# Performance work log

Measured on AMD Instinct MI355X. Metric: run time of the kernel, lower is better.

The kernel has to match this reference:

```python
import jax, jax.numpy as jnp
import numpy as np

B = 64; C = 64; DIN = 512; F = 16; S = 2; C1O = 32; C2O = 64; ND2 = 27; FC1O = 512
D = 64; CL1_F = 64; CL1_K = 5; CL2_F = 128; CL2_K = 5; FC1_F = 512; FC2_F = 2; P = 2
FC1FIN = CL2_F * (D // (P * P))  # 2048


def _conv1d(x, w, b):
    # x [B, Cin, L], w [Cout, Cin, F] -> valid conv, stride S
    y = jax.lax.conv_general_dilated(x, w, (S,), 'VALID', dimension_numbers=('NCH', 'OIH', 'NCH'))
    return y + b[None, :, None]


def _bn_c(x, g, b, eps):
    # BatchNorm1d on [B, Ch, L]: normalize each channel over (B, L) (training-mode batch stats)
    m = x.mean((0, 2), keepdims=True)
    v = ((x - m) ** 2).mean((0, 2), keepdims=True)
    return (x - m) * jax.lax.rsqrt(v + eps) * g[None, :, None] + b[None, :, None]


def _pool(x, p=2):
    # MaxPool1d(p) over last dim, floor division like torch
    L = x.shape[-1]; l = L // p
    return x[..., :l * p].reshape(x.shape[:-1] + (l, p)).max(-1)


def _branch(xc, w1, b1, g1, be1, w2, b2, g2, be2, lw, lb):
    # xc [B, 1, DIN] -> [B, FC1O]; matches max_pool(bn(relu(conv(x))), 2) twice + relu(lin1)
    o = _pool(_bn_c(jnp.maximum(_conv1d(xc, w1, b1), 0.0), g1, be1, 1e-5))
    o = _pool(_bn_c(jnp.maximum(_conv1d(o, w2, b2), 0.0), g2, be2, 1e-5))
    o = o.reshape(o.shape[0], -1)
    return jnp.maximum(o @ lw.T + lb, 0.0)


def _cheby(x, Lm, lmax, W, b, K):
    # x [B, V, Fin]; Chebyshev recursion x_k = 2 L~ x_{k-1} - x_{k-2}
    Bx, V, Fin = x.shape
    Lr = 2.0 * Lm / lmax - jnp.eye(V, dtype=x.dtype)  # rescale_L
    x0 = x.transpose(1, 2, 0).reshape(V, Fin * Bx)
    xs = [x0]
    x1 = Lr @ x0
    xs.append(x1)
    for _ in range(2, K):
        x2 = 2.0 * (Lr @ x1) - x0
        xs.append(x2)
        x0, x1 = x1, x2
    Xk = jnp.stack(xs).reshape(K, V, Fin, Bx).transpose(3, 1, 2, 0).reshape(Bx * V, Fin * K)
    return (Xk @ W.T + b).reshape(Bx, V, -1)


def _gbn(x, g, b, eps):
    # BatchNorm1d(V, eps) on [B, V, F]: per-node stats over (B, F). eps is CL1_F/CL2_F (bug in source, kept faithful)
    m = x.mean((0, 2), keepdims=True)
    v = ((x - m) ** 2).mean((0, 2), keepdims=True)
    return (x - m) * jax.lax.rsqrt(v + eps) * g[None, :, None] + b[None, :, None]


def _gpool(x):
    # graph_max_pool p=2 over node dim
    Bx, V, Fo = x.shape
    return x.reshape(Bx, V // 2, 2, Fo).max(2)


def _forward(inp, L0, L1, conv1_w, conv1_b, bn1_g, bn1_b, conv2_w, conv2_b, bn2_g, bn2_b,
             lin1_w, lin1_b, cl1_w, cl1_b, gbn1_g, gbn1_b, cl2_w, cl2_b, gbn2_g, gbn2_b,
             fc1_w, fc1_b, fc2_w, fc2_b, perm, lmax0, lmax1):
    xc = inp.transpose(1, 0, 2)[:, :, None, :]  # [C, B, 1, DIN]
    cout = jax.vmap(_branch)(xc, conv1_w, conv1_b, bn1_g, bn1_b,
                             conv2_w, conv2_b, bn2_g, bn2_b, lin1_w, lin1_b)  # [C, B, FC1O]
    x = cout[perm].transpose(1, 0, 2)  # perm_data + permute -> [B, D, FC1O]
    x = _cheby(x, L0, float(lmax0), cl1_w, cl1_b, CL1_K)
    x = _gbn(jnp.maximum(x, 0.0), gbn1_g, gbn1_b, float(CL1_F))
    x = _gpool(x)  # [B, D//2, CL1_F]
    x = _cheby(x, L1, float(lmax1), cl2_w, cl2_b, CL2_K)
    x = _gbn(jnp.maximum(x, 0.0), gbn2_g, gbn2_b, float(CL2_F))
    x = _gpool(x)  # [B, D//4, CL2_F]
    x = x.reshape(-1, FC1FIN)
    x = jnp.maximum(x @ fc1_w.T + fc1_b, 0.0)
    # Dropout(d) with d=0 is identity
    return x @ fc2_w.T + fc2_b  # [B, FC2_F]


def setup_inputs() -> dict:
    key = jax.random.key(0)
    ks = jax.random.split(key, 12)
    n = lambda k, shp: jax.random.normal(k, shp, jnp.float32) * 0.02
    A0 = jax.random.normal(ks[0], (D, D), jnp.float32); L0 = (A0 + A0.T) / 2.0
    A1 = jax.random.normal(ks[1], (D // 2, D // 2), jnp.float32); L1 = (A1 + A1.T) / 2.0
    return dict(
        inp=jax.random.normal(ks[2], (B, C, DIN), jnp.float32),
        d=0, L0=L0, L1=L1, lmax0=2, lmax1=2,
        perm=jnp.arange(D, dtype=jnp.int32), epoch_num=0,
        conv1_w=n(ks[3], (C, C1O, 1, F)), conv1_b=jnp.zeros((C, C1O), jnp.float32),
        bn1_g=jnp.ones((C, C1O), jnp.float32), bn1_b=jnp.zeros((C, C1O), jnp.float32),
        conv2_w=n(ks[4], (C, C2O, C1O, F)), conv2_b=jnp.zeros((C, C2O), jnp.float32),
        bn2_g=jnp.ones((C, C2O), jnp.float32), bn2_b=jnp.zeros((C, C2O), jnp.float32),
        lin1_w=n(ks[5], (C, FC1O, C2O * ND2)), lin1_b=jnp.zeros((C, FC1O), jnp.float32),
        cl1_w=n(ks[6], (CL1_F, CL1_K * FC1O)), cl1_b=jnp.zeros((CL1_F,), jnp.float32),
        gbn1_g=jnp.ones((D,), jnp.float32), gbn1_b=jnp.zeros((D,), jnp.float32),
        cl2_w=n(ks[7], (CL2_F, CL2_K * CL1_F)), cl2_b=jnp.zeros((CL2_F,), jnp.float32),
        gbn2_g=jnp.ones((D // 2,), jnp.float32), gbn2_b=jnp.zeros((D // 2,), jnp.float32),
        fc1_w=n(ks[8], (FC1_F, FC1FIN)), fc1_b=jnp.zeros((FC1_F,), jnp.float32),
        fc2_w=n(ks[9], (FC2_F, FC1_F)), fc2_b=jnp.zeros((FC2_F,), jnp.float32))


def reference(inp, d, L0, L1, lmax0, lmax1, perm, epoch_num,
              conv1_w, conv1_b, bn1_g, bn1_b, conv2_w, conv2_b, bn2_g, bn2_b,
              lin1_w, lin1_b, cl1_w, cl1_b, gbn1_g, gbn1_b, cl2_w, cl2_b, gbn2_g, gbn2_b,
              fc1_w, fc1_b, fc2_w, fc2_b):
    return _forward(inp, L0, L1, conv1_w, conv1_b, bn1_g, bn1_b, conv2_w, conv2_b, bn2_g, bn2_b,
                    lin1_w, lin1_b, cl1_w, cl1_b, gbn1_g, gbn1_b, cl2_w, cl2_b, gbn2_g, gbn2_b,
                    fc1_w, fc1_b, fc2_w, fc2_b, perm, lmax0, lmax1)
```

## Files before the change

### kernel.cpp

```cpp
#include <hip/hip_runtime.h>
#include <hip/hip_bf16.h>

typedef __attribute__((ext_vector_type(8))) short short8;
typedef __attribute__((ext_vector_type(4))) float f32x4;

namespace {
constexpr int Bn  = 64;
constexpr int Cn  = 64;
constexpr int C1O = 32, C2O = 64;
constexpr int L1O = 249, L1P = 124;
constexpr int L2O = 55,  L2P = 27;
constexpr int FIN1 = 512;
constexpr int LIN1K = C2O * L2P;

constexpr long S1S = 0;
constexpr long S1Q = 2048;
constexpr long S2S = 4096;
constexpr long S2Q = 8192;

constexpr long LR0_B  = 65536;
constexpr long LR1_B  = 81920;
constexpr long W1RB_B = 86016;
constexpr long W2RB_B = 413696;
constexpr long W2B_B  = 495616;
constexpr long P1B_B  = 4689920;
constexpr long Y2_B   = 37195776;
constexpr long QB_B   = 94867456;
constexpr long CO_B   = 109023232;
constexpr long XK_B   = 4689920;
constexpr long CH1_B  = 117411840;
constexpr long X2K_B  = 118460416;
constexpr long CH2_B  = 118984704;
constexpr long FCI_B  = 120033280;
constexpr long FO1_B  = 120295424;
}

__device__ __forceinline__ unsigned short f2bf(float f) {
    union { float f; unsigned u; } v; v.f = f;
    unsigned r = v.u + 0x7FFFu + ((v.u >> 16) & 1u);
    return (unsigned short)(r >> 16);
}
__device__ __forceinline__ float bf2f(unsigned short s) {
    union { unsigned u; float f; } v; v.u = ((unsigned)s) << 16;
    return v.f;
}
__device__ __forceinline__ short8 cvt8(float4 a, float4 b) {
    float f[8] = {a.x, a.y, a.z, a.w, b.x, b.y, b.z, b.w};
    union { unsigned short s[8]; short8 v; } r;
#pragma unroll
    for (int i = 0; i < 8; ++i) r.s[i] = f2bf(f[i]);
    return r.v;
}
__device__ __forceinline__ uint2 pack4(float4 a) {
    union { unsigned short s[4]; uint2 u; } r;
    r.s[0] = f2bf(a.x); r.s[1] = f2bf(a.y); r.s[2] = f2bf(a.z); r.s[3] = f2bf(a.w);
    return r.u;
}

__global__ void prep_kernel(const float* __restrict__ L0, const float* __restrict__ L1m,
                            const int* __restrict__ lmax0, const int* __restrict__ lmax1,
                            const float* __restrict__ cl1w, const float* __restrict__ cl2w,
                            const float* __restrict__ conv2w, float* __restrict__ ws)
{
    long idx = (long)blockIdx.x * 256 + threadIdx.x;
    float inv0 = 2.0f / (float)lmax0[0];
    float inv1 = 2.0f / (float)lmax1[0];
    char* wsb = (char*)ws;
    float* LR0p = (float*)(wsb + LR0_B);
    float* LR1p = (float*)(wsb + LR1_B);
    unsigned short* W1Rp = (unsigned short*)(wsb + W1RB_B);
    unsigned short* W2Rp = (unsigned short*)(wsb + W2RB_B);
    unsigned short* w2b  = (unsigned short*)(wsb + W2B_B);
    if (idx < 12288) {
        ws[idx] = 0.f;
    } else if (idx < 12288 + 4096) {
        long t = idx - 12288; int i = t / 64, j = t % 64;
        LR0p[t] = L0[t] * inv0 - (i == j ? 1.0f : 0.0f);
    } else if (idx < 12288 + 4096 + 1024) {
        long t = idx - 12288 - 4096; int i = t / 32, j = t % 32;
        LR1p[t] = L1m[t] * inv1 - (i == j ? 1.0f : 0.0f);
    } else if (idx < 12288 + 4096 + 1024 + 163840) {
        long t = idx - 12288 - 4096 - 1024;
        int k = t / 32768; int r = t % 32768; int o = r / 512, f = r % 512;
        W1Rp[t] = f2bf(cl1w[o * 2560 + f * 5 + k]);
    } else if (idx < 12288 + 4096 + 1024 + 163840 + 40960) {
        long t = idx - 12288 - 4096 - 1024 - 163840;
        int k = t / 8192; int r = t % 8192; int o = r / 64, f = r % 64;
        W2Rp[t] = f2bf(cl2w[o * 320 + f * 5 + k]);
    } else if (idx < 12288 + 4096 + 1024 + 163840 + 40960 + 2097152) {
        long t = idx - 12288 - 4096 - 1024 - 163840 - 40960;
        w2b[t] = f2bf(conv2w[t]);
    }
}

__global__ __launch_bounds__(256) void conv1_p1_kernel(const float* __restrict__ inp,
    const float* __restrict__ w1, const float* __restrict__ b1, float* __restrict__ ws)
{
    int c = blockIdx.x >> 3, bg = blockIdx.x & 7;
    __shared__ float xs[8][512];
    __shared__ float rs[8][32], rq[8][32];
    int tid = threadIdx.x;
#pragma unroll
    for (int it = 0; it < 4; ++it) {
        int f4 = it * 256 + tid;
        int bl = f4 >> 7, off = (f4 & 127) * 4;
        *(float4*)&xs[bl][off] = *(const float4*)&inp[((long)(bg * 8 + bl) * 64 + c) * 512 + off];
    }
    int o = tid & 31, bq = tid >> 5;
    int co = c * 32 + o;
    float w[16];
#pragma unroll
    for (int t = 0; t < 16; ++t) w[t] = w1[co * 16 + t];
    float bias = b1[co];
    __syncthreads();
    float s = 0.f, q = 0.f;
    for (int jg = 0; jg < 31; ++jg) {
        float x[32];
#pragma unroll
        for (int h = 0; h < 8; ++h) *(float4*)&x[h * 4] = *(const float4*)&xs[bq][jg * 16 + h * 4];
#pragma unroll
        for (int j = 0; j < 8; ++j) {
            float a = bias;
#pragma unroll
            for (int t = 0; t < 16; ++t) a = fmaf(x[2 * j + t], w[t], a);
            a = fmaxf(a, 0.f);
            s += a; q += a * a;
        }
    }
    {
        float x[16];
#pragma unroll
        for (int h = 0; h < 4; ++h) *(float4*)&x[h * 4] = *(const float4*)&xs[bq][496 + h * 4];
        float a = bias;
#pragma unroll
        for (int t = 0; t < 16; ++t) a = fmaf(x[t], w[t], a);
        a = fmaxf(a, 0.f);
        s += a; q += a * a;
    }
    rs[bq][o] = s; rq[bq][o] = q;
    __syncthreads();
    if (tid < 32) {
        float ss = 0.f, qq = 0.f;
#pragma unroll
        for (int i = 0; i < 8; ++i) { ss += rs[i][tid]; qq += rq[i][tid]; }
        atomicAdd(&ws[S1S + c * 32 + tid], ss);
        atomicAdd(&ws[S1Q + c * 32 + tid], qq);
    }
}

__global__ __launch_bounds__(256) void conv1_p2_kernel(const float* __restrict__ inp,
    const float* __restrict__ w1, const float* __restrict__ b1,
    const float* __restrict__ g, const float* __restrict__ be,
    const float* __restrict__ ws, unsigned short* __restrict__ p1)
{
    int c = blockIdx.x >> 3, bg = blockIdx.x & 7;
    __shared__ float xs[8][512];
    int tid = threadIdx.x;
#pragma unroll
    for (int it = 0; it < 4; ++it) {
        int f4 = it * 256 + tid;
        int bl = f4 >> 7, off = (f4 & 127) * 4;
        *(float4*)&xs[bl][off] = *(const float4*)&inp[((long)(bg * 8 + bl) * 64 + c) * 512 + off];
    }
    int o = tid & 31, bq = tid >> 5;
    int co = c * 32 + o;
    float w[16];
#pragma unroll
    for (int t = 0; t < 16; ++t) w[t] = w1[co * 16 + t];
    float bias = b1[co];
    float N = (float)(Bn * L1O);
    float m = ws[S1S + co] / N;
    float inv = rsqrtf(ws[S1Q + co] / N - m * m + 1e-5f);
    float sc = inv * g[co], sh = be[co] - m * sc;
    __syncthreads();
    unsigned short* op = p1 + ((long)(c * 64 + bg * 8 + bq) * 32 + o) * 124;
    for (int jg = 0; jg < 31; ++jg) {
        float x[32];
#pragma unroll
        for (int h = 0; h < 8; ++h) *(float4*)&x[h * 4] = *(const float4*)&xs[bq][jg * 16 + h * 4];
        union { unsigned short r[4]; uint2 u; } pk;
#pragma unroll
        for (int p = 0; p < 4; ++p) {
            float a0 = bias, a1 = bias;
#pragma unroll
            for (int t = 0; t < 16; ++t) {
                a0 = fmaf(x[4 * p + t], w[t], a0);
                a1 = fmaf(x[4 * p + 2 + t], w[t], a1);
            }
            float v0 = fmaxf(a0, 0.f) * sc + sh;
            float v1 = fmaxf(a1, 0.f) * sc + sh;
            pk.r[p] = f2bf(fmaxf(v0, v1));
        }
        *(uint2*)&op[jg * 4] = pk.u;
    }
}

__global__ __launch_bounds__(256) void conv2_mfma_kernel(const unsigned short* __restrict__ p1b,
    const unsigned short* __restrict__ w2b, const float* __restrict__ b2,
    unsigned short* __restrict__ y2b, float* __restrict__ s2s, float* __restrict__ s2q)
{
    int c = blockIdx.y;
    int m0 = blockIdx.x * 128;
    __shared__ unsigned short Bl[64 * 512];
    __shared__ float red[2][4][64];
    int tid = threadIdx.x;
    int w = tid >> 6, lane = tid & 63;
    int lx = lane & 15, g = lane >> 4;

    const unsigned short* wsrc = w2b + (long)c * 32768;
#pragma unroll
    for (int it = 0; it < 16; ++it) {
        int j = it * 256 + tid;
        int n = j >> 6, kb = j & 63;
        uint4 val = *(const uint4*)(wsrc + n * 512 + kb * 8);
        int dst = (n * 1024 + kb * 16) ^ ((n & 7) << 4);
        *(uint4*)((char*)Bl + dst) = val;
    }
    __syncthreads();

    const unsigned short* abase[2];
#pragma unroll
    for (int ma = 0; ma < 2; ++ma) {
        int m = m0 + w * 32 + ma * 16 + lx;
        m = min(m, 3519);
        int b = m / 55, lp = m % 55;
        abase[ma] = p1b + ((long)(c * 64 + b) * 32) * 124 + 2 * lp + (g & 1) * 8;
    }
    int cio = g >> 1;

    f32x4 acc[2][4] = {};
    for (int kstep = 0; kstep < 16; ++kstep) {
        short8 af[2];
#pragma unroll
        for (int ma = 0; ma < 2; ++ma) {
            const unsigned short* ap = abase[ma] + (kstep * 2 + cio) * 124;
            union { unsigned u[4]; short8 v; } t;
            t.u[0] = *(const unsigned*)(ap + 0);
            t.u[1] = *(const unsigned*)(ap + 2);
            t.u[2] = *(const unsigned*)(ap + 4);
            t.u[3] = *(const unsigned*)(ap + 6);
            af[ma] = t.v;
        }
#pragma unroll
        for (int fi = 0; fi < 4; ++fi) {
            int n = fi * 16 + lx;
            int off = (n * 1024 + kstep * 64 + g * 16) ^ ((n & 7) << 4);
            short8 bfrag = *(const short8*)((char*)Bl + off);
#pragma unroll
            for (int ma = 0; ma < 2; ++ma)
                acc[ma][fi] = __builtin_amdgcn_mfma_f32_16x16x32_bf16(af[ma], bfrag, acc[ma][fi], 0, 0, 0);
        }
    }

    float cs[4] = {}, cq[4] = {};
#pragma unroll
    for (int fi = 0; fi < 4; ++fi) {
        int o2 = fi * 16 + lx;
        float bia = b2[c * 64 + o2];
#pragma unroll
        for (int ma = 0; ma < 2; ++ma) {
#pragma unroll
            for (int r = 0; r < 4; ++r) {
                int mm = m0 + w * 32 + ma * 16 + g * 4 + r;
                if (mm < 3520) {
                    int bb = mm / 55, ll = mm % 55;
                    float y = fmaxf(acc[ma][fi][r] + bia, 0.f);
                    y2b[((long)(c * 64 + bb) * 55 + ll) * 64 + o2] = f2bf(y);
                    cs[fi] += y; cq[fi] += y * y;
                }
            }
        }
    }
#pragma unroll
    for (int fi = 0; fi < 4; ++fi) {
        cs[fi] += __shfl_xor(cs[fi], 16); cs[fi] += __shfl_xor(cs[fi], 32);
        cq[fi] += __shfl_xor(cq[fi], 16); cq[fi] += __shfl_xor(cq[fi], 32);
    }
    __syncthreads();
    if (g == 0) {
#pragma unroll
        for (int fi = 0; fi < 4; ++fi) { red[0][w][fi * 16 + lx] = cs[fi]; red[1][w][fi * 16 + lx] = cq[fi]; }
    }
    __syncthreads();
    if (tid < 64) {
        float ss = red[0][0][tid] + red[0][1][tid] + red[0][2][tid] + red[0][3][tid];
        float qq = red[1][0][tid] + red[1][1][tid] + red[1][2][tid] + red[1][3][tid];
        atomicAdd(&s2s[c * 64 + tid], ss);
        atomicAdd(&s2q[c * 64 + tid], qq);
    }
}

__global__ __launch_bounds__(256) void bn2_pool_kernel(const unsigned short* __restrict__ y2b,
    const float* __restrict__ ws, const float* __restrict__ g, const float* __restrict__ be,
    unsigned short* __restrict__ q)
{
    int bid = blockIdx.x;
// ... 91 lines not shown
        float acc[8][4] = {};
        for (int u = 0; u < 64; ++u) {
            float4 xv = *(const float4*)&prev[u][cg * 4];
            float4 l0 = *(const float4*)&Lt[u * 64 + vg * 8];
            float4 l1 = *(const float4*)&Lt[u * 64 + vg * 8 + 4];
            float lv[8] = {l0.x, l0.y, l0.z, l0.w, l1.x, l1.y, l1.z, l1.w};
#pragma unroll
            for (int i = 0; i < 8; ++i) {
                acc[i][0] = fmaf(lv[i], xv.x, acc[i][0]);
                acc[i][1] = fmaf(lv[i], xv.y, acc[i][1]);
                acc[i][2] = fmaf(lv[i], xv.z, acc[i][2]);
                acc[i][3] = fmaf(lv[i], xv.w, acc[i][3]);
            }
        }
#pragma unroll
        for (int i = 0; i < 8; ++i) {
            int v = vg * 8 + i;
            float4 r;
            if (k == 1) {
                r.x = acc[i][0]; r.y = acc[i][1]; r.z = acc[i][2]; r.w = acc[i][3];
            } else {
                float4 p = *(const float4*)&dst[v][cg * 4];
                r.x = 2.f * acc[i][0] - p.x; r.y = 2.f * acc[i][1] - p.y;
                r.z = 2.f * acc[i][2] - p.z; r.w = 2.f * acc[i][3] - p.w;
            }
            *(float4*)&dst[v][cg * 4] = r;
            *(uint2*)&xkb[(long)k * 2097152 + (long)v * 32768 + col] = pack4(r);
        }
        __syncthreads();
    }
}

__global__ __launch_bounds__(256) void cheby1_mfma_kernel(const unsigned short* __restrict__ xkb,
    const unsigned short* __restrict__ w1rb, const float* __restrict__ bias, float* __restrict__ out)
{
    int m0 = blockIdx.x * 16;
    __shared__ unsigned short Bl[64 * 512];
    int tid = threadIdx.x, wv = tid >> 6, lane = tid & 63;
    int lx = lane & 15, g = lane >> 4;
    int m = m0 + lx;
    int v = m & 63, b = m >> 6;

    f32x4 acc = {};
    for (int kc = 0; kc < 5; ++kc) {
        __syncthreads();
#pragma unroll
        for (int it = 0; it < 16; ++it) {
            int j = it * 256 + tid;
            int n = j >> 6, kb = j & 63;
            uint4 val = *(const uint4*)(w1rb + (long)kc * 32768 + n * 512 + kb * 8);
            int dst = (n * 1024 + kb * 16) ^ ((n & 7) << 4);
            *(uint4*)((char*)Bl + dst) = val;
        }
        __syncthreads();
        const unsigned short* ab = xkb + (long)(kc * 64 + v) * 32768 + b * 512 + g * 8;
        for (int kl = 0; kl < 16; ++kl) {
            short8 af = *(const short8*)(ab + kl * 32);
            int n = wv * 16 + lx;
            int off = (n * 1024 + kl * 64 + g * 16) ^ ((n & 7) << 4);
            short8 bfrag = *(const short8*)((char*)Bl + off);
            acc = __builtin_amdgcn_mfma_f32_16x16x32_bf16(af, bfrag, acc, 0, 0, 0);
        }
    }
    int o = wv * 16 + lx;
    float bia = bias[o];
#pragma unroll
    for (int r = 0; r < 4; ++r) {
        int mm = m0 + g * 4 + r;
        int vv = mm & 63, bb = mm >> 6;
        out[((long)(bb * 64 + vv)) * 64 + o] = fmaxf(acc[r] + bia, 0.f);
    }
}

template<int Fdim, int XOUT>
__global__ __launch_bounds__(256) void gbn_gpool_kernel(const float* __restrict__ y,
    const float* __restrict__ g, const float* __restrict__ be, float eps, int V, float* __restrict__ out)
{
    int j = blockIdx.x; int v0 = 2 * j;
    int tid = threadIdx.x;
    float s0 = 0.f, q0 = 0.f, s1 = 0.f, q1 = 0.f;
    int Ntot = Bn * Fdim;
    for (int idx = tid; idx < Ntot; idx += 256) {
        int b = idx / Fdim, f = idx % Fdim;
        float a = y[((long)b * V + v0) * Fdim + f];
        float c = y[((long)b * V + v0 + 1) * Fdim + f];
        s0 += a; q0 += a * a; s1 += c; q1 += c * c;
    }
    __shared__ float red[4][256];
    red[0][tid] = s0; red[1][tid] = q0; red[2][tid] = s1; red[3][tid] = q1;
    __syncthreads();
    for (int st = 128; st > 0; st >>= 1) {
        if (tid < st) {
#pragma unroll
            for (int r = 0; r < 4; ++r) red[r][tid] += red[r][tid + st];
        }
        __syncthreads();
    }
    float N = (float)Ntot;
    float m0 = red[0][0] / N, i0 = rsqrtf(red[1][0] / N - m0 * m0 + eps);
    float m1 = red[2][0] / N, i1 = rsqrtf(red[3][0] / N - m1 * m1 + eps);
    float sc0 = i0 * g[v0], sh0 = be[v0] - m0 * sc0;
    float sc1 = i1 * g[v0 + 1], sh1 = be[v0 + 1] - m1 * sc1;
    for (int idx = tid; idx < Ntot; idx += 256) {
        int b = idx / Fdim, f = idx % Fdim;
        float a = y[((long)b * V + v0) * Fdim + f];
        float c = y[((long)b * V + v0 + 1) * Fdim + f];
        float r = fmaxf(sc0 * a + sh0, sc1 * c + sh1);
        long oidx = XOUT ? ((long)j * Bn + b) * Fdim + f : ((long)b * (V / 2) + j) * Fdim + f;
        out[oidx] = r;
    }
}

__global__ __launch_bounds__(256) void gbn2_bf16_kernel(const float* __restrict__ y,
    const float* __restrict__ g, const float* __restrict__ be, unsigned short* __restrict__ out)
{
    constexpr int Fdim = 128; constexpr int V = 32;
    int j = blockIdx.x; int v0 = 2 * j;
    int tid = threadIdx.x;
    float s0 = 0.f, q0 = 0.f, s1 = 0.f, q1 = 0.f;
    int Ntot = Bn * Fdim;
    for (int idx = tid; idx < Ntot; idx += 256) {
        int b = idx / Fdim, f = idx % Fdim;
        float a = y[((long)b * V + v0) * Fdim + f];
        float c = y[((long)b * V + v0 + 1) * Fdim + f];
        s0 += a; q0 += a * a; s1 += c; q1 += c * c;
    }
    __shared__ float red[4][256];
    red[0][tid] = s0; red[1][tid] = q0; red[2][tid] = s1; red[3][tid] = q1;
    __syncthreads();
    for (int st = 128; st > 0; st >>= 1) {
        if (tid < st) {
#pragma unroll
            for (int r = 0; r < 4; ++r) red[r][tid] += red[r][tid + st];
        }
        __syncthreads();
    }
    float N = (float)Ntot;
    float m0 = red[0][0] / N, i0 = rsqrtf(red[1][0] / N - m0 * m0 + 128.0f);
    float m1 = red[2][0] / N, i1 = rsqrtf(red[3][0] / N - m1 * m1 + 128.0f);
    float sc0 = i0 * g[v0], sh0 = be[v0] - m0 * sc0;
    float sc1 = i1 * g[v0 + 1], sh1 = be[v0 + 1] - m1 * sc1;
    for (int idx = tid; idx < Ntot; idx += 256) {
        int b = idx / Fdim, f = idx % Fdim;
        float a = y[((long)b * V + v0) * Fdim + f];
        float c = y[((long)b * V + v0 + 1) * Fdim + f];
        float r = fmaxf(sc0 * a + sh0, sc1 * c + sh1);
        out[((long)b * 16 + j) * Fdim + f] = f2bf(r);
    }
}

__global__ __launch_bounds__(256) void layer2_kernel(const float* __restrict__ x2k0,
    const float* __restrict__ Lr1, const unsigned short* __restrict__ w2rb,
    const float* __restrict__ bias, float* __restrict__ out)
{
    int b = blockIdx.x;
    __shared__ float xs[5][32][72];
    __shared__ unsigned short wsl[128 * 320];
    int tid = threadIdx.x;
#pragma unroll
    for (int it = 0; it < 20; ++it) {
        int j = it * 256 + tid;
        int o = j / 40, kb = j % 40;
        uint4 val = *(const uint4*)(w2rb + ((long)(kb >> 3) * 128 + o) * 64 + (kb & 7) * 8);
        int dst = (o * 640 + kb * 16) ^ ((o & 7) << 4);
        *(uint4*)((char*)wsl + dst) = val;
    }
    int v = tid & 31, fg = tid >> 5;
    float lrow[32];
#pragma unroll
    for (int u = 0; u < 32; ++u) lrow[u] = Lr1[v * 32 + u];
    {
        const float* sp = x2k0 + ((long)v * 64 + b) * 64 + fg * 8;
        float4 a = *(const float4*)sp;
        float4 c = *(const float4*)(sp + 4);
        *(float4*)&xs[0][v][fg * 8] = a;
        *(float4*)&xs[0][v][fg * 8 + 4] = c;
    }
    __syncthreads();
    for (int k = 1; k < 5; ++k) {
        float acc[8] = {};
#pragma unroll
        for (int u = 0; u < 32; ++u) {
            float4 xa = *(const float4*)&xs[k - 1][u][fg * 8];
            float4 xb = *(const float4*)&xs[k - 1][u][fg * 8 + 4];
            float l = lrow[u];
            acc[0] = fmaf(l, xa.x, acc[0]); acc[1] = fmaf(l, xa.y, acc[1]);
            acc[2] = fmaf(l, xa.z, acc[2]); acc[3] = fmaf(l, xa.w, acc[3]);
            acc[4] = fmaf(l, xb.x, acc[4]); acc[5] = fmaf(l, xb.y, acc[5]);
            acc[6] = fmaf(l, xb.z, acc[6]); acc[7] = fmaf(l, xb.w, acc[7]);
        }
        float4 ra, rb;
        if (k >= 2) {
            float4 pa = *(const float4*)&xs[k - 2][v][fg * 8];
            float4 pb = *(const float4*)&xs[k - 2][v][fg * 8 + 4];
            ra.x = 2.f * acc[0] - pa.x; ra.y = 2.f * acc[1] - pa.y;
            ra.z = 2.f * acc[2] - pa.z; ra.w = 2.f * acc[3] - pa.w;
            rb.x = 2.f * acc[4] - pb.x; rb.y = 2.f * acc[5] - pb.y;
            rb.z = 2.f * acc[6] - pb.z; rb.w = 2.f * acc[7] - pb.w;
        } else {
            ra.x = acc[0]; ra.y = acc[1]; ra.z = acc[2]; ra.w = acc[3];
            rb.x = acc[4]; rb.y = acc[5]; rb.z = acc[6]; rb.w = acc[7];
        }
        *(float4*)&xs[k][v][fg * 8] = ra;
        *(float4*)&xs[k][v][fg * 8 + 4] = rb;
        __syncthreads();
    }
    int wv = tid >> 6, lane = tid & 63;
    int lx = lane & 15, g = lane >> 4;
    f32x4 acc2[2][2] = {};
    for (int kstep = 0; kstep < 10; ++kstep) {
        int k = kstep * 32 + g * 8;
        int kc = k >> 6, f = k & 63;
        short8 af[2];
#pragma unroll
        for (int ma = 0; ma < 2; ++ma) {
            int vv = ma * 16 + lx;
            float4 xa = *(const float4*)&xs[kc][vv][f];
            float4 xb = *(const float4*)&xs[kc][vv][f + 4];
            af[ma] = cvt8(xa, xb);
        }
#pragma unroll
        for (int nb = 0; nb < 2; ++nb) {
            int o = wv * 32 + nb * 16 + lx;
            int kb = kstep * 4 + g;
            int off = (o * 640 + kb * 16) ^ ((o & 7) << 4);
            short8 bf = *(const short8*)((char*)wsl + off);
#pragma unroll
            for (int ma = 0; ma < 2; ++ma)
                acc2[ma][nb] = __builtin_amdgcn_mfma_f32_16x16x32_bf16(af[ma], bf, acc2[ma][nb], 0, 0, 0);
        }
    }
#pragma unroll
    for (int ma = 0; ma < 2; ++ma)
#pragma unroll
        for (int nb = 0; nb < 2; ++nb) {
            int o = wv * 32 + nb * 16 + lx;
            float bia = bias[o];
#pragma unroll
            for (int r = 0; r < 4; ++r) {
                int vv = ma * 16 + g * 4 + r;
                out[((long)b * 32 + vv) * 128 + o] = fmaxf(acc2[ma][nb][r] + bia, 0.f);
            }
        }
}

__global__ void fc2_kernel(const float* __restrict__ x, const float* __restrict__ w,
                           const float* __restrict__ bv, float* __restrict__ out)
{
    int tid = threadIdx.x;
    int b = tid >> 1, o = tid & 1;
    float acc = bv[o];
    for (int f = 0; f < 512; ++f) acc = fmaf(x[b * 512 + f], w[o * 512 + f], acc);
    out[tid] = acc;
}

extern "C" void kernel_launch(void* const* d_in, const int* in_sizes, int n_in,
                              void* d_out, int out_size, void* d_ws, size_t ws_size,
                              hipStream_t stream)
{
    const float* inp    = (const float*)d_in[0];
    const float* L0     = (const float*)d_in[2];
    const float* L1m    = (const float*)d_in[3];
    const int*   lmax0  = (const int*)d_in[4];
    const int*   lmax1  = (const int*)d_in[5];
    const int*   perm   = (const int*)d_in[6];
    const float* conv1_w = (const float*)d_in[8];
    const float* conv1_b = (const float*)d_in[9];
    const float* bn1_g  = (const float*)d_in[10];
    const float* bn1_b  = (const float*)d_in[11];
    const float* conv2_w = (const float*)d_in[12];
    const float* conv2_b = (const float*)d_in[13];
    const float* bn2_g  = (const float*)d_in[14];
    const float* bn2_b  = (const float*)d_in[15];
    const float* lin1_w = (const float*)d_in[16];
    const float* lin1_b = (const float*)d_in[17];
    const float* cl1_w  = (const float*)d_in[18];
    const float* cl1_b  = (const float*)d_in[19];
    const float* gbn1_g = (const float*)d_in[20];
    const float* gbn1_b = (const float*)d_in[21];
    const float* cl2_w  = (const float*)d_in[22];
    const float* cl2_b  = (const float*)d_in[23];
    const float* gbn2_g = (const float*)d_in[24];
    const float* gbn2_b = (const float*)d_in[25];
    const float* fc1_w  = (const float*)d_in[26];
    const float* fc1_b  = (const float*)d_in[27];
    const float* fc2_w  = (const float*)d_in[28];
    const float* fc2_b  = (const float*)d_in[29];
    float* ws  = (float*)d_ws;
    char*  wsb = (char*)d_ws;
    float* out = (float*)d_out;

    unsigned short* w1rb = (unsigned short*)(wsb + W1RB_B);
    unsigned short* w2rb = (unsigned short*)(wsb + W2RB_B);
    unsigned short* w2b  = (unsigned short*)(wsb + W2B_B);
    unsigned short* p1b  = (unsigned short*)(wsb + P1B_B);
    unsigned short* y2b  = (unsigned short*)(wsb + Y2_B);
    unsigned short* qb   = (unsigned short*)(wsb + QB_B);
    float*          co   = (float*)(wsb + CO_B);
    unsigned short* xkb  = (unsigned short*)(wsb + XK_B);
    float*          ch1  = (float*)(wsb + CH1_B);
    float*          x2k0 = (float*)(wsb + X2K_B);
    float*          ch2  = (float*)(wsb + CH2_B);
    unsigned short* fci  = (unsigned short*)(wsb + FCI_B);
    float*          fo1  = (float*)(wsb + FO1_B);
    float*          lr0  = (float*)(wsb + LR0_B);
    float*          lr1  = (float*)(wsb + LR1_B);

    prep_kernel<<<9060, 256, 0, stream>>>(L0, L1m, lmax0, lmax1, cl1_w, cl2_w, conv2_w, ws);

    conv1_p1_kernel<<<512, 256, 0, stream>>>(inp, conv1_w, conv1_b, ws);
    conv1_p2_kernel<<<512, 256, 0, stream>>>(inp, conv1_w, conv1_b, bn1_g, bn1_b, ws, p1b);

    conv2_mfma_kernel<<<dim3(28, 64), 256, 0, stream>>>(p1b, w2b, conv2_b, y2b, ws + S2S, ws + S2Q);
    bn2_pool_kernel<<<4096, 256, 0, stream>>>(y2b, ws, bn2_g, bn2_b, qb);

    gemm_a16w32_kernel<<<dim3(8, 64), 256, 0, stream>>>(qb, lin1_w, lin1_b, co,
        LIN1K, 512, (long)64 * LIN1K, (long)512 * LIN1K, 512, (long)64 * 512);

    rec_fused_kernel<<<256, 256, 0, stream>>>(lr0, co, perm, xkb);
    cheby1_mfma_kernel<<<256, 256, 0, stream>>>(xkb, w1rb, cl1_b, ch1);

    gbn_gpool_kernel<64, 1><<<32, 256, 0, stream>>>(ch1, gbn1_g, gbn1_b, 64.0f, 64, x2k0);

    layer2_kernel<<<64, 256, 0, stream>>>(x2k0, lr1, w2rb, cl2_b, ch2);

    gbn2_bf16_kernel<<<16, 256, 0, stream>>>(ch2, gbn2_g, gbn2_b, fci);

    gemm_a16w32_kernel<<<dim3(8, 1), 256, 0, stream>>>(fci, fc1_w, fc1_b, fo1,
        2048, 512, 0, 0, 0, 0);
    fc2_kernel<<<1, 128, 0, stream>>>(fo1, fc2_w, fc2_b, out);
}
```

Measured before the change: 345.0 us.

## Fuse prep with conv1 stats, fold graph BN/pool into consumers, enlarge conv2 tiles

Merges the prep kernel and conv1 statistics pass into one launch, and replaces the conv1 stat atomics with per-block partial sums. Graph batch-norm statistics are now accumulated in the cheby1 and layer2 epilogues through shuffles and atomics. The normalise-and-pool steps move into the input loads of layer2 and a new fc1 MFMA kernel, which removes the two gbn kernels and the old fc1 GEMM launch. Conv2 tiles double to 256 rows per block, halving the grid and reusing each B fragment across more MFMAs. This cuts launches and intermediate global traffic, but lowers parallelism in conv2 and fc1 (8 blocks).

```diff
diff --git a/kernel.cpp b/kernel.cpp
--- a/kernel.cpp
+++ b/kernel.cpp
@@ -10,29 +10,29 @@
 constexpr int C1O = 32, C2O = 64;
 constexpr int L1O = 249, L1P = 124;
 constexpr int L2O = 55,  L2P = 27;
-constexpr int FIN1 = 512;
 constexpr int LIN1K = C2O * L2P;
 
-constexpr long S1S = 0;
-constexpr long S1Q = 2048;
-constexpr long S2S = 4096;
-constexpr long S2Q = 8192;
-
-constexpr long LR0_B  = 65536;
-constexpr long LR1_B  = 81920;
-constexpr long W1RB_B = 86016;
-constexpr long W2RB_B = 413696;
-constexpr long W2B_B  = 495616;
-constexpr long P1B_B  = 4689920;
-constexpr long Y2_B   = 37195776;
+constexpr long S2S = 0;
+constexpr long S2Q = 4096;
+constexpr long G1S = 8192;
+constexpr long G1Q = 8256;
+constexpr long G2S = 8320;
+constexpr long G2Q = 8352;
+constexpr long P1P = 8448;
+
+constexpr long LR0_B  = 165888;
+constexpr long LR1_B  = 182272;
+constexpr long W1RB_B = 186368;
+constexpr long W2RB_B = 514048;
+constexpr long W2B_B  = 595968;
+constexpr long P1B_B  = 4790272;
+constexpr long Y2_B   = 37296128;
 constexpr long QB_B   = 94867456;
 constexpr long CO_B   = 109023232;
-constexpr long XK_B   = 4689920;
+constexpr long XK_B   = 4790272;
 constexpr long CH1_B  = 117411840;
-constexpr long X2K_B  = 118460416;
-constexpr long CH2_B  = 118984704;
-constexpr long FCI_B  = 120033280;
-constexpr long FO1_B  = 120295424;
+constexpr long CH2_B  = 118460416;
+constexpr long FO1_B  = 119508992;
 }
 
 __device__ __forceinline__ unsigned short f2bf(float f) {
@@ -57,48 +57,105 @@
     return r.u;
 }
 
-__global__ void prep_kernel(const float* __restrict__ L0, const float* __restrict__ L1m,
-                            const int* __restrict__ lmax0, const int* __restrict__ lmax1,
-                            const float* __restrict__ cl1w, const float* __restrict__ cl2w,
-                            const float* __restrict__ conv2w, float* __restrict__ ws)
-{
-    long idx = (long)blockIdx.x * 256 + threadIdx.x;
-    float inv0 = 2.0f / (float)lmax0[0];
-    float inv1 = 2.0f / (float)lmax1[0];
-    char* wsb = (char*)ws;
-    float* LR0p = (float*)(wsb + LR0_B);
-    float* LR1p = (float*)(wsb + LR1_B);
-    unsigned short* W1Rp = (unsigned short*)(wsb + W1RB_B);
-    unsigned short* W2Rp = (unsigned short*)(wsb + W2RB_B);
-    unsigned short* w2b  = (unsigned short*)(wsb + W2B_B);
-    if (idx < 12288) {
-        ws[idx] = 0.f;
-    } else if (idx < 12288 + 4096) {
-        long t = idx - 12288; int i = t / 64, j = t % 64;
-        LR0p[t] = L0[t] * inv0 - (i == j ? 1.0f : 0.0f);
-    } else if (idx < 12288 + 4096 + 1024) {
-        long t = idx - 12288 - 4096; int i = t / 32, j = t % 32;
-        LR1p[t] = L1m[t] * inv1 - (i == j ? 1.0f : 0.0f);
-    } else if (idx < 12288 + 4096 + 1024 + 163840) {
-        long t = idx - 12288 - 4096 - 1024;
-        int k = t / 32768; int r = t % 32768; int o = r / 512, f = r % 512;
-        W1Rp[t] = f2bf(cl1w[o * 2560 + f * 5 + k]);
-    } else if (idx < 12288 + 4096 + 1024 + 163840 + 40960) {
-        long t = idx - 12288 - 4096 - 1024 - 163840;
-        int k = t / 8192; int r = t % 8192; int o = r / 64, f = r % 64;
-        W2Rp[t] = f2bf(cl2w[o * 320 + f * 5 + k]);
-    } else if (idx < 12288 + 4096 + 1024 + 163840 + 40960 + 2097152) {
-        long t = idx - 12288 - 4096 - 1024 - 163840 - 40960;
-        w2b[t] = f2bf(conv2w[t]);
-    }
-}
-
-__global__ __launch_bounds__(256) void conv1_p1_kernel(const float* __restrict__ inp,
-    const float* __restrict__ w1, const float* __restrict__ b1, float* __restrict__ ws)
+__global__ __launch_bounds__(256) void k1_prep_conv1_kernel(
+    const float* __restrict__ inp, const float* __restrict__ w1, const float* __restrict__ b1,
+    const float* __restrict__ L0, const float* __restrict__ L1m,
+    const int* __restrict__ lmax0, const int* __restrict__ lmax1,
+    const float* __restrict__ cl1w, const float* __restrict__ cl2w,
+    const float* __restrict__ conv2w, float* __restrict__ ws)
+{
+    int bid = blockIdx.x;
+    int tid = threadIdx.x;
+    if (bid < 512) {
+        int c = bid >> 3, bg = bid & 7;
+        __shared__ float xs[8][512];
+        __shared__ float rs[8][32], rq[8][32];
+#pragma unroll
+        for (int it = 0; it < 4; ++it) {
+            int f4 = it * 256 + tid;
+            int bl = f4 >> 7, off = (f4 & 127) * 4;
+            *(float4*)&xs[bl][off] = *(const float4*)&inp[((long)(bg * 8 + bl) * 64 + c) * 512 + off];
+        }
+        int o = tid & 31, bq = tid >> 5;
+        int co = c * 32 + o;
+        float w[16];
+#pragma unroll
+        for (int t = 0; t < 16; ++t) w[t] = w1[co * 16 + t];
+        float bias = b1[co];
+        __syncthreads();
+        float s = 0.f, q = 0.f;
+        for (int jg = 0; jg < 31; ++jg) {
+            float x[32];
+#pragma unroll
+            for (int h = 0; h < 8; ++h) *(float4*)&x[h * 4] = *(const float4*)&xs[bq][jg * 16 + h * 4];
+#pragma unroll
+            for (int j = 0; j < 8; ++j) {
+                float a = bias;
+#pragma unroll
+                for (int t = 0; t < 16; ++t) a = fmaf(x[2 * j + t], w[t], a);
+                a = fmaxf(a, 0.f);
+                s += a; q += a * a;
+            }
+        }
+        {
+            float x[16];
+#pragma unroll
+            for (int h = 0; h < 4; ++h) *(float4*)&x[h * 4] = *(const float4*)&xs[bq][496 + h * 4];
+            float a = bias;
+#pragma unroll
+            for (int t = 0; t < 16; ++t) a = fmaf(x[t], w[t], a);
+            a = fmaxf(a, 0.f);
+            s += a; q += a * a;
+        }
+        rs[bq][o] = s; rq[bq][o] = q;
+        __syncthreads();
+        if (tid < 32) {
+            float ss = 0.f, qq = 0.f;
+#pragma unroll
+            for (int i = 0; i < 8; ++i) { ss += rs[i][tid]; qq += rq[i][tid]; }
+            ws[P1P + (long)(c * 32 + tid) * 16 + bg * 2]     = ss;
+            ws[P1P + (long)(c * 32 + tid) * 16 + bg * 2 + 1] = qq;
+        }
+    } else {
+        long idx = (long)(bid - 512) * 256 + tid;
+        float inv0 = 2.0f / (float)lmax0[0];
+        float inv1 = 2.0f / (float)lmax1[0];
+        char* wsb = (char*)ws;
+        float* LR0p = (float*)(wsb + LR0_B);
+        float* LR1p = (float*)(wsb + LR1_B);
+        unsigned short* W1Rp = (unsigned short*)(wsb + W1RB_B);
+        unsigned short* W2Rp = (unsigned short*)(wsb + W2RB_B);
+        unsigned short* w2b  = (unsigned short*)(wsb + W2B_B);
+        if (idx < 8384) {
+            ws[idx] = 0.f;
+        } else if (idx < 8384 + 4096) {
+            long t = idx - 8384; int i = t / 64, j = t % 64;
+            LR0p[t] = L0[t] * inv0 - (i == j ? 1.0f : 0.0f);
+        } else if (idx < 8384 + 4096 + 1024) {
+            long t = idx - 8384 - 4096; int i = t / 32, j = t % 32;
+            LR1p[t] = L1m[t] * inv1 - (i == j ? 1.0f : 0.0f);
+        } else if (idx < 8384 + 4096 + 1024 + 163840) {
+            long t = idx - 8384 - 4096 - 1024;
+            int k = t / 32768; int r = t % 32768; int o = r / 512, f = r % 512;
+            W1Rp[t] = f2bf(cl1w[o * 2560 + f * 5 + k]);
+        } else if (idx < 8384 + 4096 + 1024 + 163840 + 40960) {
+            long t = idx - 8384 - 4096 - 1024 - 163840;
+            int k = t / 8192; int r = t % 8192; int o = r / 64, f = r % 64;
+            W2Rp[t] = f2bf(cl2w[o * 320 + f * 5 + k]);
+        } else if (idx < 8384 + 4096 + 1024 + 163840 + 40960 + 2097152) {
+            long t = idx - 8384 - 4096 - 1024 - 163840 - 40960;
+            w2b[t] = f2bf(conv2w[t]);
+        }
+    }
+}
+
+__global__ __launch_bounds__(256) void conv1_p2_kernel(const float* __restrict__ inp,
+    const float* __restrict__ w1, const float* __restrict__ b1,
+    const float* __restrict__ g, const float* __restrict__ be,
+    const float* __restrict__ ws, unsigned short* __restrict__ p1)
 {
     int c = blockIdx.x >> 3, bg = blockIdx.x & 7;
     __shared__ float xs[8][512];
-    __shared__ float rs[8][32], rq[8][32];
     int tid = threadIdx.x;
 #pragma unroll
     for (int it = 0; it < 4; ++it) {
@@ -112,65 +169,15 @@
 #pragma unroll
     for (int t = 0; t < 16; ++t) w[t] = w1[co * 16 + t];
     float bias = b1[co];
-    __syncthreads();
-    float s = 0.f, q = 0.f;
-    for (int jg = 0; jg < 31; ++jg) {
-        float x[32];
-#pragma unroll
-        for (int h = 0; h < 8; ++h) *(float4*)&x[h * 4] = *(const float4*)&xs[bq][jg * 16 + h * 4];
-#pragma unroll
-        for (int j = 0; j < 8; ++j) {
-            float a = bias;
-#pragma unroll
-            for (int t = 0; t < 16; ++t) a = fmaf(x[2 * j + t], w[t], a);
-            a = fmaxf(a, 0.f);
-            s += a; q += a * a;
-        }
-    }
-    {
-        float x[16];
-#pragma unroll
-        for (int h = 0; h < 4; ++h) *(float4*)&x[h * 4] = *(const float4*)&xs[bq][496 + h * 4];
-        float a = bias;
-#pragma unroll
-        for (int t = 0; t < 16; ++t) a = fmaf(x[t], w[t], a);
-        a = fmaxf(a, 0.f);
-        s += a; q += a * a;
-    }
-    rs[bq][o] = s; rq[bq][o] = q;
-    __syncthreads();
-    if (tid < 32) {
-        float ss = 0.f, qq = 0.f;
-#pragma unroll
-        for (int i = 0; i < 8; ++i) { ss += rs[i][tid]; qq += rq[i][tid]; }
-        atomicAdd(&ws[S1S + c * 32 + tid], ss);
-        atomicAdd(&ws[S1Q + c * 32 + tid], qq);
-    }
-}
-
-__global__ __launch_bounds__(256) void conv1_p2_kernel(const float* __restrict__ inp,
-    const float* __restrict__ w1, const float* __restrict__ b1,
-    const float* __restrict__ g, const float* __restrict__ be,
-    const float* __restrict__ ws, unsigned short* __restrict__ p1)
-{
-    int c = blockIdx.x >> 3, bg = blockIdx.x & 7;
-    __shared__ float xs[8][512];
-    int tid = threadIdx.x;
-#pragma unroll
-    for (int it = 0; it < 4; ++it) {
-        int f4 = it * 256 + tid;
-        int bl = f4 >> 7, off = (f4 & 127) * 4;
-        *(float4*)&xs[bl][off] = *(const float4*)&inp[((long)(bg * 8 + bl) * 64 + c) * 512 + off];
-    }
-    int o = tid & 31, bq = tid >> 5;
-    int co = c * 32 + o;
-    float w[16];
-#pragma unroll
-    for (int t = 0; t < 16; ++t) w[t] = w1[co * 16 + t];
-    float bias = b1[co];
+    float ssum = 0.f, qsum = 0.f;
+#pragma unroll
+    for (int i = 0; i < 8; ++i) {
+        ssum += ws[P1P + (long)co * 16 + i * 2];
+        qsum += ws[P1P + (long)co * 16 + i * 2 + 1];
+    }
     float N = (float)(Bn * L1O);
-    float m = ws[S1S + co] / N;
-    float inv = rsqrtf(ws[S1Q + co] / N - m * m + 1e-5f);
+    float m = ssum / N;
+    float inv = rsqrtf(qsum / N - m * m + 1e-5f);
     float sc = inv * g[co], sh = be[co] - m * sc;
     __syncthreads();
     unsigned short* op = p1 + ((long)(c * 64 + bg * 8 + bq) * 32 + o) * 124;
@@ -200,7 +207,7 @@
     unsigned short* __restrict__ y2b, float* __restrict__ s2s, float* __restrict__ s2q)
 {
     int c = blockIdx.y;
-    int m0 = blockIdx.x * 128;
+    int m0 = blockIdx.x * 256;
     __shared__ unsigned short Bl[64 * 512];
     __shared__ float red[2][4][64];
     int tid = threadIdx.x;
@@ -218,21 +225,21 @@
     }
     __syncthreads();
 
-    const unsigned short* abase[2];
-#pragma unroll
-    for (int ma = 0; ma < 2; ++ma) {
-        int m = m0 + w * 32 + ma * 16 + lx;
+    const unsigned short* abase[4];
+#pragma unroll
+    for (int ma = 0; ma < 4; ++ma) {
+        int m = m0 + w * 64 + ma * 16 + lx;
         m = min(m, 3519);
         int b = m / 55, lp = m % 55;
         abase[ma] = p1b + ((long)(c * 64 + b) * 32) * 124 + 2 * lp + (g & 1) * 8;
     }
     int cio = g >> 1;
 
-    f32x4 acc[2][4] = {};
+    f32x4 acc[4][4] = {};
     for (int kstep = 0; kstep < 16; ++kstep) {
-        short8 af[2];
-#pragma unroll
-        for (int ma = 0; ma < 2; ++ma) {
+        short8 af[4];
+#pragma unroll
+        for (int ma = 0; ma < 4; ++ma) {
             const unsigned short* ap = abase[ma] + (kstep * 2 + cio) * 124;
             union { unsigned u[4]; short8 v; } t;
             t.u[0] = *(const unsigned*)(ap + 0);
@@ -247,7 +254,7 @@
             int off = (n * 1024 + kstep * 64 + g * 16) ^ ((n & 7) << 4);
             short8 bfrag = *(const short8*)((char*)Bl + off);
 #pragma unroll
-            for (int ma = 0; ma < 2; ++ma)
+            for (int ma = 0; ma < 4; ++ma)
                 acc[ma][fi] = __builtin_amdgcn_mfma_f32_16x16x32_bf16(af[ma], bfrag, acc[ma][fi], 0, 0, 0);
         }
     }
@@ -258,10 +265,10 @@
         int o2 = fi * 16 + lx;
         float bia = b2[c * 64 + o2];
 #pragma unroll
-        for (int ma = 0; ma < 2; ++ma) {
+        for (int ma = 0; ma < 4; ++ma) {
 #pragma unroll
             for (int r = 0; r < 4; ++r) {
-                int mm = m0 + w * 32 + ma * 16 + g * 4 + r;
+                int mm = m0 + w * 64 + ma * 16 + g * 4 + r;
                 if (mm < 3520) {
                     int bb = mm / 55, ll = mm % 55;
                     float y = fmaxf(acc[ma][fi][r] + bia, 0.f);
@@ -419,10 +426,12 @@
 }
 
 __global__ __launch_bounds__(256) void cheby1_mfma_kernel(const unsigned short* __restrict__ xkb,
-    const unsigned short* __restrict__ w1rb, const float* __restrict__ bias, float* __restrict__ out)
+    const unsigned short* __restrict__ w1rb, const float* __restrict__ bias,
+    float* __restrict__ out, float* __restrict__ g1s, float* __restrict__ g1q)
 {
     int m0 = blockIdx.x * 16;
     __shared__ unsigned short Bl[64 * 512];
+    __shared__ float rS[4][16], rQ[4][16];
     int tid = threadIdx.x, wv = tid >> 6, lane = tid & 63;
     int lx = lane & 15, g = lane >> 4;
     int m = m0 + lx;
@@ -451,98 +460,48 @@
     }
     int o = wv * 16 + lx;
     float bia = bias[o];
+    float sv[4], qv[4];
 #pragma unroll
     for (int r = 0; r < 4; ++r) {
         int mm = m0 + g * 4 + r;
         int vv = mm & 63, bb = mm >> 6;
-        out[((long)(bb * 64 + vv)) * 64 + o] = fmaxf(acc[r] + bia, 0.f);
-    }
-}
-
-template<int Fdim, int XOUT>
-__global__ __launch_bounds__(256) void gbn_gpool_kernel(const float* __restrict__ y,
-    const float* __restrict__ g, const float* __restrict__ be, float eps, int V, float* __restrict__ out)
-{
-    int j = blockIdx.x; int v0 = 2 * j;
-    int tid = threadIdx.x;
-    float s0 = 0.f, q0 = 0.f, s1 = 0.f, q1 = 0.f;
-    int Ntot = Bn * Fdim;
-    for (int idx = tid; idx < Ntot; idx += 256) {
-        int b = idx / Fdim, f = idx % Fdim;
-        float a = y[((long)b * V + v0) * Fdim + f];
-        float c = y[((long)b * V + v0 + 1) * Fdim + f];
-        s0 += a; q0 += a * a; s1 += c; q1 += c * c;
-    }
-    __shared__ float red[4][256];
-    red[0][tid] = s0; red[1][tid] = q0; red[2][tid] = s1; red[3][tid] = q1;
-    __syncthreads();
-    for (int st = 128; st > 0; st >>= 1) {
-        if (tid < st) {
-#pragma unroll
-            for (int r = 0; r < 4; ++r) red[r][tid] += red[r][tid + st];
-        }
-        __syncthreads();
-    }
-    float N = (float)Ntot;
-    float m0 = red[0][0] / N, i0 = rsqrtf(red[1][0] / N - m0 * m0 + eps);
-    float m1 = red[2][0] / N, i1 = rsqrtf(red[3][0] / N - m1 * m1 + eps);
-    float sc0 = i0 * g[v0], sh0 = be[v0] - m0 * sc0;
-    float sc1 = i1 * g[v0 + 1], sh1 = be[v0 + 1] - m1 * sc1;
-    for (int idx = tid; idx < Ntot; idx += 256) {
-        int b = idx / Fdim, f = idx % Fdim;
-        float a = y[((long)b * V + v0) * Fdim + f];
-        float c = y[((long)b * V + v0 + 1) * Fdim + f];
-        float r = fmaxf(sc0 * a + sh0, sc1 * c + sh1);
-        long oidx = XOUT ? ((long)j * Bn + b) * Fdim + f : ((long)b * (V / 2) + j) * Fdim + f;
-        out[oidx] = r;
-    }
-}
-
-__global__ __launch_bounds__(256) void gbn2_bf16_kernel(const float* __restrict__ y,
-    const float* __restrict__ g, const float* __restrict__ be, unsigned short* __restrict__ out)
-{
-    constexpr int Fdim = 128; constexpr int V = 32;
-    int j = blockIdx.x; int v0 = 2 * j;
-    int tid = threadIdx.x;
-    float s0 = 0.f, q0 = 0.f, s1 = 0.f, q1 = 0.f;
-    int Ntot = Bn * Fdim;
-    for (int idx = tid; idx < Ntot; idx += 256) {
-        int b = idx / Fdim, f = idx % Fdim;
-        float a = y[((long)b * V + v0) * Fdim + f];
-        float c = y[((long)b * V + v0 + 1) * Fdim + f];
-        s0 += a; q0 += a * a; s1 += c; q1 += c * c;
-    }
-    __shared__ float red[4][256];
-    red[0][tid] = s0; red[1][tid] = q0; red[2][tid] = s1; red[3][tid] = q1;
-    __syncthreads();
-    for (int st = 128; st > 0; st >>= 1) {
-        if (tid < st) {
-#pragma unroll
-            for (int r = 0; r < 4; ++r) red[r][tid] += red[r][tid + st];
-        }
-        __syncthreads();
-    }
-    float N = (float)Ntot;
-    float m0 = red[0][0] / N, i0 = rsqrtf(red[1][0] / N - m0 * m0 + 128.0f);
-    float m1 = red[2][0] / N, i1 = rsqrtf(red[3][0] / N - m1 * m1 + 128.0f);
-    float sc0 = i0 * g[v0], sh0 = be[v0] - m0 * sc0;
-    float sc1 = i1 * g[v0 + 1], sh1 = be[v0 + 1] - m1 * sc1;
-    for (int idx = tid; idx < Ntot; idx += 256) {
-        int b = idx / Fdim, f = idx % Fdim;
-        float a = y[((long)b * V + v0) * Fdim + f];
-        float c = y[((long)b * V + v0 + 1) * Fdim + f];
-        float r = fmaxf(sc0 * a + sh0, sc1 * c + sh1);
-        out[((long)b * 16 + j) * Fdim + f] = f2bf(r);
-    }
-}
-
-__global__ __launch_bounds__(256) void layer2_kernel(const float* __restrict__ x2k0,
+        float val = fmaxf(acc[r] + bia, 0.f);
+        out[((long)(bb * 64 + vv)) * 64 + o] = val;
+        sv[r] = val; qv[r] = val * val;
+    }
+#pragma unroll
+    for (int r = 0; r < 4; ++r) {
+#pragma unroll
+        for (int msk = 1; msk < 16; msk <<= 1) {
+            sv[r] += __shfl_xor(sv[r], msk);
+            qv[r] += __shfl_xor(qv[r], msk);
+        }
+    }
+    if (lx == 0) {
+#pragma unroll
+        for (int r = 0; r < 4; ++r) { rS[wv][g * 4 + r] = sv[r]; rQ[wv][g * 4 + r] = qv[r]; }
+    }
+    __syncthreads();
+    if (tid < 16) {
+        float ss = rS[0][tid] + rS[1][tid] + rS[2][tid] + rS[3][tid];
+        float qq = rQ[0][tid] + rQ[1][tid] + rQ[2][tid] + rQ[3][tid];
+        int vv = (m0 + tid) & 63;
+        atomicAdd(&g1s[vv], ss);
+        atomicAdd(&g1q[vv], qq);
+    }
+}
+
+__global__ __launch_bounds__(256) void layer2_kernel(const float* __restrict__ ch1,
+    const float* __restrict__ g1s, const float* __restrict__ g1q,
+    const float* __restrict__ gbn1g, const float* __restrict__ gbn1b,
     const float* __restrict__ Lr1, const unsigned short* __restrict__ w2rb,
-    const float* __restrict__ bias, float* __restrict__ out)
+    const float* __restrict__ bias, float* __restrict__ out,
+    float* __restrict__ g2s, float* __restrict__ g2q)
 {
     int b = blockIdx.x;
     __shared__ float xs[5][32][72];
     __shared__ unsigned short wsl[128 * 320];
+    __shared__ float r2S[4][32], r2Q[4][32];
     int tid = threadIdx.x;
 #pragma unroll
     for (int it = 0; it < 20; ++it) {
@@ -557,11 +516,29 @@
 #pragma unroll
     for (int u = 0; u < 32; ++u) lrow[u] = Lr1[v * 32 + u];
     {
-        const float* sp = x2k0 + ((long)v * 64 + b) * 64 + fg * 8;
-        float4 a = *(const float4*)sp;
-        float4 c = *(const float4*)(sp + 4);
-        *(float4*)&xs[0][v][fg * 8] = a;
-        *(float4*)&xs[0][v][fg * 8 + 4] = c;
+        float N1 = 4096.f;
+        float mA = g1s[2 * v] / N1;
+        float iA = rsqrtf(g1q[2 * v] / N1 - mA * mA + 64.0f);
+        float mB = g1s[2 * v + 1] / N1;
+        float iB = rsqrtf(g1q[2 * v + 1] / N1 - mB * mB + 64.0f);
+        float sc0 = iA * gbn1g[2 * v], sh0 = gbn1b[2 * v] - mA * sc0;
+        float sc1 = iB * gbn1g[2 * v + 1], sh1 = gbn1b[2 * v + 1] - mB * sc1;
+        const float* c0 = ch1 + ((long)b * 64 + 2 * v) * 64 + fg * 8;
+        float4 a0 = *(const float4*)c0;
+        float4 a1 = *(const float4*)(c0 + 4);
+        float4 b0 = *(const float4*)(c0 + 64);
+        float4 b1 = *(const float4*)(c0 + 68);
+        float4 r0, r1;
+        r0.x = fmaxf(sc0 * a0.x + sh0, sc1 * b0.x + sh1);
+        r0.y = fmaxf(sc0 * a0.y + sh0, sc1 * b0.y + sh1);
+        r0.z = fmaxf(sc0 * a0.z + sh0, sc1 * b0.z + sh1);
+        r0.w = fmaxf(sc0 * a0.w + sh0, sc1 * b0.w + sh1);
+        r1.x = fmaxf(sc0 * a1.x + sh0, sc1 * b1.x + sh1);
+        r1.y = fmaxf(sc0 * a1.y + sh0, sc1 * b1.y + sh1);
+        r1.z = fmaxf(sc0 * a1.z + sh0, sc1 * b1.z + sh1);
+        r1.w = fmaxf(sc0 * a1.w + sh0, sc1 * b1.w + sh1);
+        *(float4*)&xs[0][v][fg * 8] = r0;
+        *(float4*)&xs[0][v][fg * 8 + 4] = r1;
     }
     __syncthreads();
     for (int k = 1; k < 5; ++k) {
@@ -617,6 +594,7 @@
                 acc2[ma][nb] = __builtin_amdgcn_mfma_f32_16x16x32_bf16(af[ma], bf, acc2[ma][nb], 0, 0, 0);
         }
     }
+    float s2[2][4] = {}, q2[2][4] = {};
 #pragma unroll
     for (int ma = 0; ma < 2; ++ma)
 #pragma unroll
@@ -626,7 +604,106 @@
 #pragma unroll
             for (int r = 0; r < 4; ++r) {
                 int vv = ma * 16 + g * 4 + r;
-                out[((long)b * 32 + vv) * 128 + o] = fmaxf(acc2[ma][nb][r] + bia, 0.f);
+                float val = fmaxf(acc2[ma][nb][r] + bia, 0.f);
+                out[((long)b * 32 + vv) * 128 + o] = val;
+                s2[ma][r] += val; q2[ma][r] += val * val;
+            }
+        }
+#pragma unroll
+    for (int ma = 0; ma < 2; ++ma)
+#pragma unroll
+        for (int r = 0; r < 4; ++r) {
+#pragma unroll
+            for (int msk = 1; msk < 16; msk <<= 1) {
+                s2[ma][r] += __shfl_xor(s2[ma][r], msk);
+                q2[ma][r] += __shfl_xor(q2[ma][r], msk);
+            }
+        }
+    if (lx == 0) {
+#pragma unroll
+        for (int ma = 0; ma < 2; ++ma)
+#pragma unroll
+            for (int r = 0; r < 4; ++r) {
+                r2S[wv][ma * 16 + g * 4 + r] = s2[ma][r];
+                r2Q[wv][ma * 16 + g * 4 + r] = q2[ma][r];
+            }
+    }
+    __syncthreads();
+    if (tid < 32) {
+        float ss = r2S[0][tid] + r2S[1][tid] + r2S[2][tid] + r2S[3][tid];
+        float qq = r2Q[0][tid] + r2Q[1][tid] + r2Q[2][tid] + r2Q[3][tid];
+        atomicAdd(&g2s[tid], ss);
+        atomicAdd(&g2q[tid], qq);
+    }
+}
+
+__global__ __launch_bounds__(256) void fc1_kernel(const float* __restrict__ ch2,
+    const float* __restrict__ g2s, const float* __restrict__ g2q,
+    const float* __restrict__ gg, const float* __restrict__ gb,
+    const float* __restrict__ W, const float* __restrict__ bias, float* __restrict__ C)
+{
+    int n0 = blockIdx.x * 64;
+    int tid = threadIdx.x, wv = tid >> 6, lane = tid & 63;
+    int lx = lane & 15, g = lane >> 4;
+    int wm = wv & 1, wn = wv >> 1;
+
+    const float* w0 = W + (long)(n0 + wn * 32 + lx) * 2048 + g * 8;
+
+    f32x4 acc[2][2] = {};
+    for (int kstep = 0; kstep < 64; ++kstep) {
+        int k = kstep * 32 + g * 8;
+        int j = k >> 7, f0 = k & 127;
+        float N2 = 8192.f;
+        float m0_ = g2s[2 * j] / N2;
+        float i0 = rsqrtf(g2q[2 * j] / N2 - m0_ * m0_ + 128.0f);
+        float m1_ = g2s[2 * j + 1] / N2;
+        float i1 = rsqrtf(g2q[2 * j + 1] / N2 - m1_ * m1_ + 128.0f);
+        float sc0 = i0 * gg[2 * j], sh0 = gb[2 * j] - m0_ * sc0;
+        float sc1 = i1 * gg[2 * j + 1], sh1 = gb[2 * j + 1] - m1_ * sc1;
+        short8 af[2];
+#pragma unroll
+        for (int ma = 0; ma < 2; ++ma) {
+            int b = wm * 32 + ma * 16 + lx;
+            const float* p = ch2 + ((long)b * 32 + 2 * j) * 128 + f0;
+            float4 x0 = *(const float4*)p;
+            float4 x1 = *(const float4*)(p + 4);
+            float4 y0 = *(const float4*)(p + 128);
+            float4 y1 = *(const float4*)(p + 132);
+            float4 r0, r1;
+            r0.x = fmaxf(sc0 * x0.x + sh0, sc1 * y0.x + sh1);
+            r0.y = fmaxf(sc0 * x0.y + sh0, sc1 * y0.y + sh1);
+            r0.z = fmaxf(sc0 * x0.z + sh0, sc1 * y0.z + sh1);
+            r0.w = fmaxf(sc0 * x0.w + sh0, sc1 * y0.w + sh1);
+            r1.x = fmaxf(sc0 * x1.x + sh0, sc1 * y1.x + sh1);
+            r1.y = fmaxf(sc0 * x1.y + sh0, sc1 * y1.y + sh1);
+            r1.z = fmaxf(sc0 * x1.z + sh0, sc1 * y1.z + sh1);
+            r1.w = fmaxf(sc0 * x1.w + sh0, sc1 * y1.w + sh1);
+            af[ma] = cvt8(r0, r1);
+        }
+        short8 bf[2];
+#pragma unroll
+        for (int nb = 0; nb < 2; ++nb) {
+            const float* wp = w0 + (long)nb * 16 * 2048 + kstep * 32;
+            float4 x = *(const float4*)(wp);
+            float4 y = *(const float4*)(wp + 4);
+            bf[nb] = cvt8(x, y);
+        }
+#pragma unroll
+        for (int ma = 0; ma < 2; ++ma)
+#pragma unroll
+            for (int nb = 0; nb < 2; ++nb)
+                acc[ma][nb] = __builtin_amdgcn_mfma_f32_16x16x32_bf16(af[ma], bf[nb], acc[ma][nb], 0, 0, 0);
+    }
+#pragma unroll
+    for (int ma = 0; ma < 2; ++ma)
+#pragma unroll
+        for (int nb = 0; nb < 2; ++nb) {
+            int o = n0 + wn * 32 + nb * 16 + lx;
+            float bia = bias[o];
+#pragma unroll
+            for (int r = 0; r < 4; ++r) {
+                int b = wm * 32 + ma * 16 + g * 4 + r;
+                C[(long)b * 512 + o] = fmaxf(acc[ma][nb][r] + bia, 0.f);
             }
         }
 }
@@ -686,34 +763,32 @@
     float*          co   = (float*)(wsb + CO_B);
     unsigned short* xkb  = (unsigned short*)(wsb + XK_B);
     float*          ch1  = (float*)(wsb + CH1_B);
-    float*          x2k0 = (float*)(wsb + X2K_B);
     float*          ch2  = (float*)(wsb + CH2_B);
-    unsigned short* fci  = (unsigned short*)(wsb + FCI_B);
     float*          fo1  = (float*)(wsb + FO1_B);
     float*          lr0  = (float*)(wsb + LR0_B);
     float*          lr1  = (float*)(wsb + LR1_B);
 
-    prep_kernel<<<9060, 256, 0, stream>>>(L0, L1m, lmax0, lmax1, cl1_w, cl2_w, conv2_w, ws);
-
-    conv1_p1_kernel<<<512, 256, 0, stream>>>(inp, conv1_w, conv1_b, ws);
+    k1_prep_conv1_kernel<<<9557, 256, 0, stream>>>(inp, conv1_w, conv1_b,
+        L0, L1m, lmax0, lmax1, cl1_w, cl2_w, conv2_w, ws);
+
     conv1_p2_kernel<<<512, 256, 0, stream>>>(inp, conv1_w, conv1_b, bn1_g, bn1_b, ws, p1b);
 
-    conv2_mfma_kernel<<<dim3(28, 64), 256, 0, stream>>>(p1b, w2b, conv2_b, y2b, ws + S2S, ws + S2Q);
+    conv2_mfma_kernel<<<dim3(14, 64), 256, 0, stream>>>(p1b, w2b, conv2_b, y2b, ws + S2S, ws + S2Q);
+
     bn2_pool_kernel<<<4096, 256, 0, stream>>>(y2b, ws, bn2_g, bn2_b, qb);
 
     gemm_a16w32_kernel<<<dim3(8, 64), 256, 0, stream>>>(qb, lin1_w, lin1_b, co,
         LIN1K, 512, (long)64 * LIN1K, (long)512 * LIN1K, 512, (long)64 * 512);
 
     rec_fused_kernel<<<256, 256, 0, stream>>>(lr0, co, perm, xkb);
-    cheby1_mfma_kernel<<<256, 256, 0, stream>>>(xkb, w1rb, cl1_b, ch1);
-
-    gbn_gpool_kernel<64, 1><<<32, 256, 0, stream>>>(ch1, gbn1_g, gbn1_b, 64.0f, 64, x2k0);
-
-    layer2_kernel<<<64, 256, 0, stream>>>(x2k0, lr1, w2rb, cl2_b, ch2);
-
-    gbn2_bf16_kernel<<<16, 256, 0, stream>>>(ch2, gbn2_g, gbn2_b, fci);
-
-    gemm_a16w32_kernel<<<dim3(8, 1), 256, 0, stream>>>(fci, fc1_w, fc1_b, fo1,
-        2048, 512, 0, 0, 0, 0);
+
+    cheby1_mfma_kernel<<<256, 256, 0, stream>>>(xkb, w1rb, cl1_b, ch1, ws + G1S, ws + G1Q);
+
+    layer2_kernel<<<64, 256, 0, stream>>>(ch1, ws + G1S, ws + G1Q, gbn1_g, gbn1_b,
+        lr1, w2rb, cl2_b, ch2, ws + G2S, ws + G2Q);
+
+    fc1_kernel<<<8, 256, 0, stream>>>(ch2, ws + G2S, ws + G2Q, gbn2_g, gbn2_b,
+        fc1_w, fc1_b, fo1);
+
     fc2_kernel<<<1, 128, 0, stream>>>(fo1, fc2_w, fc2_b, out);
 }
```

Measured after the change: 364.5 us. +5.6%, slower.
